# Performance work log

Measured on AMD Instinct MI355X. Metric: run time of the kernel, lower is better.

The kernel has to match this reference:

```python
import jax, jax.numpy as jnp
import numpy as np

L, B, S, D, H, F = 8, 8, 2048, 1024, 16, 4096
DH = D // H
EPS = 1e-5


def setup_inputs() -> dict:
    key = jax.random.key(0)
    ks = jax.random.split(key, 8)
    sc = 0.02
    return {
        "x": jax.random.normal(ks[0], (B, S, D), jnp.float32),
        "layer_indices": jax.random.randint(ks[1], (B,), 0, L, jnp.int32),
        "Wq": jax.random.normal(ks[2], (L, D, D), jnp.float32) * sc,
        "bq": jnp.zeros((L, D), jnp.float32),
        "Wk": jax.random.normal(ks[3], (L, D, D), jnp.float32) * sc,
        "bk": jnp.zeros((L, D), jnp.float32),
        "Wv": jax.random.normal(ks[4], (L, D, D), jnp.float32) * sc,
        "bv": jnp.zeros((L, D), jnp.float32),
        "Wo": jax.random.normal(ks[5], (L, D, D), jnp.float32) * sc,
        "bo": jnp.zeros((L, D), jnp.float32),
        "ln1_s": jnp.ones((L, D), jnp.float32),
        "ln1_b": jnp.zeros((L, D), jnp.float32),
        "ln2_s": jnp.ones((L, D), jnp.float32),
        "ln2_b": jnp.zeros((L, D), jnp.float32),
        "W1": jax.random.normal(ks[6], (L, D, F), jnp.float32) * sc,
        "b1": jnp.zeros((L, F), jnp.float32),
        "W2": jax.random.normal(ks[7], (L, F, D), jnp.float32) * sc,
        "b2": jnp.zeros((L, D), jnp.float32),
    }


def _layernorm(x, s, b):
    # x: [B,S,D]; s,b: [B,D] (per-routed-layer params)
    m = jnp.mean(x, axis=-1, keepdims=True)
    v = jnp.mean(jnp.square(x - m), axis=-1, keepdims=True)
    return (x - m) * jax.lax.rsqrt(v + EPS) * s[:, None, :] + b[:, None, :]


def reference(x, layer_indices, Wq, bq, Wk, bk, Wv, bv, Wo, bo,
              ln1_s, ln1_b, ln2_s, ln2_b, W1, b1, W2, b2):
    idx = layer_indices
    # Gather each batch element's routed layer parameters (MoE-style dispatch).
    Wq_g, bq_g = Wq[idx], bq[idx]
    Wk_g, bk_g = Wk[idx], bk[idx]
    Wv_g, bv_g = Wv[idx], bv[idx]
    Wo_g, bo_g = Wo[idx], bo[idx]
    s1, b1n = ln1_s[idx], ln1_b[idx]
    s2, b2n = ln2_s[idx], ln2_b[idx]
    W1_g, bf1 = W1[idx], b1[idx]
    W2_g, bf2 = W2[idx], b2[idx]

    # --- Multi-head self-attention (pre-LN) ---
    h = _layernorm(x, s1, b1n)                                   # [B,S,D]
    q = jnp.einsum('bsd,bde->bse', h, Wq_g) + bq_g[:, None, :]
    k = jnp.einsum('bsd,bde->bse', h, Wk_g) + bk_g[:, None, :]
    v = jnp.einsum('bsd,bde->bse', h, Wv_g) + bv_g[:, None, :]
    q = q.reshape(B, S, H, DH)
    k = k.reshape(B, S, H, DH)
    v = v.reshape(B, S, H, DH)
    scores = jnp.einsum('bqhd,bkhd->bhqk', q, k) / np.sqrt(DH)   # [B,H,S,S]
    probs = jax.nn.softmax(scores, axis=-1)
    attn = jnp.einsum('bhqk,bkhd->bqhd', probs, v).reshape(B, S, D)
    attn = jnp.einsum('bsd,bde->bse', attn, Wo_g) + bo_g[:, None, :]
    x = x + attn

    # --- Feed-forward (pre-LN) ---
    h = _layernorm(x, s2, b2n)
    h = jax.nn.gelu(jnp.einsum('bsd,bdf->bsf', h, W1_g) + bf1[:, None, :])
    h = jnp.einsum('bsf,bfd->bsd', h, W2_g) + bf2[:, None, :]
    return x + h
```

## Files before the change

kernel.cpp:

```cpp
#include <hip/hip_runtime.h>
#include <cstdint>
#include <cstddef>

typedef __attribute__((ext_vector_type(8))) short s8v;
typedef __attribute__((ext_vector_type(4))) float f4v;

constexpr int Lc = 8, Bc = 8, Sc = 2048, Dc = 1024, Hc = 16, Fc = 4096;

__device__ __forceinline__ unsigned short f2bf(float f) {
    unsigned int u = __float_as_uint(f);
    u = (u + 0x7FFFu + ((u >> 16) & 1u)) >> 16;
    return (unsigned short)u;
}

__device__ __forceinline__ void gload_lds16(const unsigned short* g, unsigned short* l) {
    __builtin_amdgcn_global_load_lds(
        (__attribute__((address_space(1))) void*)g,
        (__attribute__((address_space(3))) void*)l,
        16, 0, 0);
}

__global__ __launch_bounds__(256) void transpose_cast(
    const float* __restrict__ in, unsigned short* __restrict__ out, int R, int C) {
    __shared__ float tile[32][33];
    int l = blockIdx.z;
    int r0 = blockIdx.y << 5, c0 = blockIdx.x << 5;
    const float* ip = in + (size_t)l * R * C;
    unsigned short* op = out + (size_t)l * R * C;
    int tx = threadIdx.x & 31, ty = threadIdx.x >> 5;
#pragma unroll
    for (int i = 0; i < 4; i++)
        tile[ty + i * 8][tx] = ip[(size_t)(r0 + ty + i * 8) * C + (c0 + tx)];
    __syncthreads();
#pragma unroll
    for (int i = 0; i < 4; i++)
        op[(size_t)(c0 + ty + i * 8) * R + (r0 + tx)] = f2bf(tile[tx][ty + i * 8]);
}

__global__ __launch_bounds__(256) void ln_kernel(
    const float* __restrict__ x, const float* __restrict__ sc, const float* __restrict__ bi,
    const int* __restrict__ idx, unsigned short* __restrict__ out) {
    int row = blockIdx.x;
    int b = row >> 11;
    int l = idx[b];
    const float* xr = x + (size_t)row * Dc;
    int t = threadIdx.x;
    float4 xv = *(const float4*)(xr + t * 4);
    float s = xv.x + xv.y + xv.z + xv.w;
    float ss = xv.x * xv.x + xv.y * xv.y + xv.z * xv.z + xv.w * xv.w;
#pragma unroll
    for (int off = 32; off; off >>= 1) { s += __shfl_xor(s, off); ss += __shfl_xor(ss, off); }
    __shared__ float red[2][4];
    int w = t >> 6, lane = t & 63;
    if (lane == 0) { red[0][w] = s; red[1][w] = ss; }
    __syncthreads();
    float tot = red[0][0] + red[0][1] + red[0][2] + red[0][3];
    float tots = red[1][0] + red[1][1] + red[1][2] + red[1][3];
    float mean = tot * (1.0f / Dc);
    float var = tots * (1.0f / Dc) - mean * mean;
    float r = rsqrtf(var + 1e-5f);
    float4 s4 = *(const float4*)(sc + (size_t)l * Dc + t * 4);
    float4 b4 = *(const float4*)(bi + (size_t)l * Dc + t * 4);
    ushort4 o;
    o.x = f2bf((xv.x - mean) * r * s4.x + b4.x);
    o.y = f2bf((xv.y - mean) * r * s4.y + b4.y);
    o.z = f2bf((xv.z - mean) * r * s4.z + b4.z);
    o.w = f2bf((xv.w - mean) * r * s4.w + b4.w);
    *(ushort4*)(out + (size_t)row * Dc + t * 4) = o;
}

template <int EPI>
__global__ __launch_bounds__(256) void gemm_kernel(
    const unsigned short* __restrict__ A, const unsigned short* __restrict__ Wt,
    const float* __restrict__ bias, const int* __restrict__ idx,
    const float* __restrict__ resid, void* __restrict__ out, int M, int N, int K) {
    int b = blockIdx.z;
    int l = idx[b];
    int m0 = blockIdx.y << 7, n0 = blockIdx.x << 7;
    const unsigned short* Ab = A + (size_t)b * M * K;
    const unsigned short* Wl = Wt + (size_t)l * N * K;
    __shared__ alignas(16) unsigned short As[128][32];
    __shared__ alignas(16) unsigned short Bs[128][32];
    int tid = threadIdx.x, w = tid >> 6, lane = tid & 63, quad = lane >> 4, lr = lane & 15;
    int wm = (w >> 1) << 6, wn = (w & 1) << 6;
    f4v acc[4][4];
#pragma unroll
    for (int i = 0; i < 4; i++)
#pragma unroll
        for (int j = 0; j < 4; j++) acc[i][j] = 0.f;

    int chrow = 32 * w + (lane >> 2);
    int ks = (lane & 3) * 8;
    const unsigned short* agp0 = Ab + (size_t)(m0 + chrow) * K + ks;
    const unsigned short* agp1 = agp0 + (size_t)16 * K;
    const unsigned short* bgp0 = Wl + (size_t)(n0 + chrow) * K + ks;
    const unsigned short* bgp1 = bgp0 + (size_t)16 * K;
    unsigned short* lA0 = &As[32 * w][0];
    unsigned short* lA1 = &As[32 * w + 16][0];
    unsigned short* lB0 = &Bs[32 * w][0];
    unsigned short* lB1 = &Bs[32 * w + 16][0];

    for (int k0 = 0; k0 < K; k0 += 32) {
        gload_lds16(agp0, lA0);
        gload_lds16(agp1, lA1);
        gload_lds16(bgp0, lB0);
        gload_lds16(bgp1, lB1);
        agp0 += 32; agp1 += 32; bgp0 += 32; bgp1 += 32;
        __syncthreads();
        s8v af[4], bf[4];
#pragma unroll
        for (int i = 0; i < 4; i++) af[i] = *(const s8v*)&As[wm + i * 16 + lr][quad * 8];
#pragma unroll
        for (int j = 0; j < 4; j++) bf[j] = *(const s8v*)&Bs[wn + j * 16 + lr][quad * 8];
#pragma unroll
        for (int i = 0; i < 4; i++)
#pragma unroll
            for (int j = 0; j < 4; j++)
                acc[i][j] = __builtin_amdgcn_mfma_f32_16x16x32_bf16(af[i], bf[j], acc[i][j], 0, 0, 0);
        __syncthreads();
    }

    float bj[4];
#pragma unroll
    for (int j = 0; j < 4; j++) bj[j] = bias[(size_t)l * N + (n0 + wn + j * 16 + lr)];
    size_t obase = (size_t)b * M * N;
#pragma unroll
    for (int i = 0; i < 4; i++) {
#pragma unroll
        for (int r = 0; r < 4; r++) {
            int gm = m0 + wm + i * 16 + quad * 4 + r;
            size_t rowoff = obase + (size_t)gm * N;
#pragma unroll
            for (int j = 0; j < 4; j++) {
                int gn = n0 + wn + j * 16 + lr;
                float val = acc[i][j][r] + bj[j];
                if constexpr (EPI == 0) {
                    ((unsigned short*)out)[rowoff + gn] = f2bf(val);
                } else if constexpr (EPI == 1) {
                    float g = 0.5f * val * (1.0f + tanhf(0.7978845608f * (val + 0.044715f * val * val * val)));
                    ((unsigned short*)out)[rowoff + gn] = f2bf(g);
                } else {
                    ((float*)out)[rowoff + gn] = resid[rowoff + gn] + val;
                }
            }
        }
    }
}

__global__ __launch_bounds__(256) void flash_kernel(
    const unsigned short* __restrict__ qm, const unsigned short* __restrict__ km,
    const unsigned short* __restrict__ vm, unsigned short* __restrict__ om) {
    const int b = blockIdx.z, h = blockIdx.y, q0 = blockIdx.x << 6;
    const int tid = threadIdx.x, w = tid >> 6, lane = tid & 63, quad = lane >> 4, lr = lane & 15;
    __shared__ alignas(16) unsigned short Pl[4][16][72];
    __shared__ alignas(16) unsigned short Vt[64][72];
    const size_t bS = (size_t)b * Sc;
    const int hoff = h << 6;

    s8v aq0, aq1;
    {
        const unsigned short* qr = qm + (bS + q0 + w * 16 + lr) * (size_t)Dc + hoff;
        aq0 = *(const s8v*)(qr + quad * 8);
        aq1 = *(const s8v*)(qr + 32 + quad * 8);
    }
    f4v accO[4];
#pragma unroll
    for (int i = 0; i < 4; i++) accO[i] = 0.f;
    float m_i[4] = {-3e38f, -3e38f, -3e38f, -3e38f};
    float l_i[4] = {0.f, 0.f, 0.f, 0.f};

    const int vkey = tid >> 2, vc = tid & 3;

    for (int kv0 = 0; kv0 < Sc; kv0 += 64) {
        const unsigned short* vp = vm + (bS + kv0 + vkey) * (size_t)Dc + hoff + vc * 16;
        s8v v0 = *(const s8v*)vp;
        s8v v1 = *(const s8v*)(vp + 8);
        __syncthreads();
#pragma unroll
        for (int e = 0; e < 8; e++) {
            Vt[vc * 16 + e][vkey] = (unsigned short)v0[e];
            Vt[vc * 16 + 8 + e][vkey] = (unsigned short)v1[e];
        }
        f4v sc4[4];
#pragma unroll
        for (int j = 0; j < 4; j++) {
            const unsigned short* kr = km + (bS + kv0 + j * 16 + lr) * (size_t)Dc + hoff;
            s8v b0 = *(const s8v*)(kr + quad * 8);
            s8v b1 = *(const s8v*)(kr + 32 + quad * 8);
            f4v c = 0.f;
            c = __builtin_amdgcn_mfma_f32_16x16x32_bf16(aq0, b0, c, 0, 0, 0);
            c = __builtin_amdgcn_mfma_f32_16x16x32_bf16(aq1, b1, c, 0, 0, 0);
            sc4[j] = c * 0.125f;
        }
        float alpha[4], pmat[4][4];
#pragma unroll
        for (int rr = 0; rr < 4; rr++) {
            float lm = fmaxf(fmaxf(sc4[0][rr], sc4[1][rr]), fmaxf(sc4[2][rr], sc4[3][rr]));
#pragma unroll
            for (int off = 1; off < 16; off <<= 1) lm = fmaxf(lm, __shfl_xor(lm, off));
            float mn = fmaxf(m_i[rr], lm);
            alpha[rr] = __expf(m_i[rr] - mn);
            m_i[rr] = mn;
            float ls = 0.f;
#pragma unroll
            for (int j = 0; j < 4; j++) {
                float p = __expf(sc4[j][rr] - mn);
                pmat[j][rr] = p;
                ls += p;
            }
#pragma unroll
            for (int off = 1; off < 16; off <<= 1) ls += __shfl_xor(ls, off);
            l_i[rr] = l_i[rr] * alpha[rr] + ls;
        }
#pragma unroll
        for (int jd = 0; jd < 4; jd++)
#pragma unroll
            for (int rr = 0; rr < 4; rr++) accO[jd][rr] *= alpha[rr];
#pragma unroll
        for (int j = 0; j < 4; j++)
#pragma unroll
            for (int rr = 0; rr < 4; rr++)
                Pl[w][quad * 4 + rr][j * 16 + lr] = f2bf(pmat[j][rr]);
        __syncthreads();
        s8v ap0 = *(const s8v*)&Pl[w][lr][quad * 8];
        s8v ap1 = *(const s8v*)&Pl[w][lr][32 + quad * 8];
#pragma unroll
        for (int jd = 0; jd < 4; jd++) {
            s8v b0 = *(const s8v*)&Vt[jd * 16 + lr][quad * 8];
            s8v b1 = *(const s8v*)&Vt[jd * 16 + lr][32 + quad * 8];
            accO[jd] = __builtin_amdgcn_mfma_f32_16x16x32_bf16(ap0, b0, accO[jd], 0, 0, 0);
            accO[jd] = __builtin_amdgcn_mfma_f32_16x16x32_bf16(ap1, b1, accO[jd], 0, 0, 0);
        }
    }
#pragma unroll
    for (int jd = 0; jd < 4; jd++)
#pragma unroll
        for (int rr = 0; rr < 4; rr++)
            om[(bS + q0 + w * 16 + quad * 4 + rr) * (size_t)Dc + hoff + jd * 16 + lr] =
                f2bf(accO[jd][rr] / l_i[rr]);
}

extern "C" void kernel_launch(void* const* d_in, const int* in_sizes, int n_in,
                              void* d_out, int out_size, void* d_ws, size_t ws_size,
                              hipStream_t stream) {
    const float* x  = (const float*)d_in[0];
    const int* idx  = (const int*)d_in[1];
    const float* Wq = (const float*)d_in[2];  const float* bq  = (const float*)d_in[3];
    const float* Wk = (const float*)d_in[4];  const float* bk  = (const float*)d_in[5];
    const float* Wv = (const float*)d_in[6];  const float* bv  = (const float*)d_in[7];
    const float* Wo = (const float*)d_in[8];  const float* bo  = (const float*)d_in[9];
    const float* s1 = (const float*)d_in[10]; const float* b1n = (const float*)d_in[11];
    const float* s2 = (const float*)d_in[12]; const float* b2n = (const float*)d_in[13];
    const float* W1 = (const float*)d_in[14]; const float* bf1 = (const float*)d_in[15];
    const float* W2 = (const float*)d_in[16]; const float* bf2 = (const float*)d_in[17];

    const size_t eDD  = (size_t)Lc * Dc * Dc;
    const size_t eDF  = (size_t)Lc * Dc * Fc;
    const size_t eBSD = (size_t)Bc * Sc * Dc;
    unsigned short* Wtq = (unsigned short*)d_ws;
    unsigned short* Wtk = Wtq + eDD;
    unsigned short* Wtv = Wtk + eDD;
    unsigned short* Wto = Wtv + eDD;
    unsigned short* Wt1 = Wto + eDD;
    unsigned short* Wt2 = Wt1 + eDF;
    unsigned short* hb  = Wt2 + eDF;
    unsigned short* qb  = hb + eBSD;
    unsigned short* kb  = qb + eBSD;
    unsigned short* vb  = kb + eBSD;
    unsigned short* ab  = vb + eBSD;
    float* x2           = (float*)(ab + eBSD);
    unsigned short* fb  = qb;

    dim3 blk(256);
    transpose_cast<<<dim3(Dc / 32, Dc / 32, Lc), blk, 0, stream>>>(Wq, Wtq, Dc, Dc);
    transpose_cast<<<dim3(Dc / 32, Dc / 32, Lc), blk, 0, stream>>>(Wk, Wtk, Dc, Dc);
    transpose_cast<<<dim3(Dc / 32, Dc / 32, Lc), blk, 0, stream>>>(Wv, Wtv, Dc, Dc);
    transpose_cast<<<dim3(Dc / 32, Dc / 32, Lc), blk, 0, stream>>>(Wo, Wto, Dc, Dc);
    transpose_cast<<<dim3(Fc / 32, Dc / 32, Lc), blk, 0, stream>>>(W1, Wt1, Dc, Fc);
    transpose_cast<<<dim3(Dc / 32, Fc / 32, Lc), blk, 0, stream>>>(W2, Wt2, Fc, Dc);
    ln_kernel<<<Bc * Sc, blk, 0, stream>>>(x, s1, b1n, idx, hb);
    gemm_kernel<0><<<dim3(Dc / 128, Sc / 128, Bc), blk, 0, stream>>>(hb, Wtq, bq, idx, nullptr, qb, Sc, Dc, Dc);
    gemm_kernel<0><<<dim3(Dc / 128, Sc / 128, Bc), blk, 0, stream>>>(hb, Wtk, bk, idx, nullptr, kb, Sc, Dc, Dc);
    gemm_kernel<0><<<dim3(Dc / 128, Sc / 128, Bc), blk, 0, stream>>>(hb, Wtv, bv, idx, nullptr, vb, Sc, Dc, Dc);
    flash_kernel<<<dim3(Sc / 64, Hc, Bc), blk, 0, stream>>>(qb, kb, vb, ab);
    gemm_kernel<2><<<dim3(Dc / 128, Sc / 128, Bc), blk, 0, stream>>>(ab, Wto, bo, idx, x, x2, Sc, Dc, Dc);
    ln_kernel<<<Bc * Sc, blk, 0, stream>>>(x2, s2, b2n, idx, hb);
    gemm_kernel<1><<<dim3(Fc / 128, Sc / 128, Bc), blk, 0, stream>>>(hb, Wt1, bf1, idx, nullptr, fb, Sc, Fc, Dc);
    gemm_kernel<2><<<dim3(Dc / 128, Sc / 128, Bc), blk, 0, stream>>>(fb, Wt2, bf2, idx, x2, (float*)d_out, Sc, Dc, Fc);
}
```

Baseline: 1.789 ms.

## Produce V transposed from its projection GEMM and read it directly in flash attention

The V projection GEMM now runs with the weight as the left operand, so V is written head-dim-major ([B, D, S]) and the bias is applied per output row. The flash kernel then loads the V operand straight from global memory in MFMA layout, which removes the per-tile LDS transpose and the two block-wide barriers. The cost is that V fragments are read from global/L2 by every wave rather than once per block into shared memory, and the V GEMM's epilogue stores run along S.

New measurement: 2.141 ms. +19.7%, slower.

```diff
diff --git a/kernel.cpp b/kernel.cpp
--- a/kernel.cpp
+++ b/kernel.cpp
@@ -69,7 +69,7 @@
     *(ushort4*)(out + (size_t)row * Dc + t * 4) = o;
 }
 
-template <int EPI>
+template <int EPI, bool WLEFT = false>
 __global__ __launch_bounds__(256) void gemm_kernel(
     const unsigned short* __restrict__ A, const unsigned short* __restrict__ Wt,
     const float* __restrict__ bias, const int* __restrict__ idx,
@@ -77,8 +77,8 @@
     int b = blockIdx.z;
     int l = idx[b];
     int m0 = blockIdx.y << 7, n0 = blockIdx.x << 7;
-    const unsigned short* Ab = A + (size_t)b * M * K;
-    const unsigned short* Wl = Wt + (size_t)l * N * K;
+    const unsigned short* Ab = A + (WLEFT ? (size_t)l : (size_t)b) * M * K;
+    const unsigned short* Wl = Wt + (WLEFT ? (size_t)b : (size_t)l) * N * K;
     __shared__ alignas(16) unsigned short As[128][32];
     __shared__ alignas(16) unsigned short Bs[128][32];
     int tid = threadIdx.x, w = tid >> 6, lane = tid & 63, quad = lane >> 4, lr = lane & 15;
@@ -121,8 +121,10 @@
     }
 
     float bj[4];
-#pragma unroll
-    for (int j = 0; j < 4; j++) bj[j] = bias[(size_t)l * N + (n0 + wn + j * 16 + lr)];
+    if constexpr (!WLEFT) {
+#pragma unroll
+        for (int j = 0; j < 4; j++) bj[j] = bias[(size_t)l * N + (n0 + wn + j * 16 + lr)];
+    }
     size_t obase = (size_t)b * M * N;
 #pragma unroll
     for (int i = 0; i < 4; i++) {
@@ -130,10 +132,12 @@
         for (int r = 0; r < 4; r++) {
             int gm = m0 + wm + i * 16 + quad * 4 + r;
             size_t rowoff = obase + (size_t)gm * N;
+            float bm;
+            if constexpr (WLEFT) bm = bias[(size_t)l * M + gm];
 #pragma unroll
             for (int j = 0; j < 4; j++) {
                 int gn = n0 + wn + j * 16 + lr;
-                float val = acc[i][j][r] + bj[j];
+                float val = acc[i][j][r] + (WLEFT ? bm : bj[j]);
                 if constexpr (EPI == 0) {
                     ((unsigned short*)out)[rowoff + gn] = f2bf(val);
                 } else if constexpr (EPI == 1) {
@@ -153,9 +157,9 @@
     const int b = blockIdx.z, h = blockIdx.y, q0 = blockIdx.x << 6;
     const int tid = threadIdx.x, w = tid >> 6, lane = tid & 63, quad = lane >> 4, lr = lane & 15;
     __shared__ alignas(16) unsigned short Pl[4][16][72];
-    __shared__ alignas(16) unsigned short Vt[64][72];
     const size_t bS = (size_t)b * Sc;
     const int hoff = h << 6;
+    const unsigned short* vtb = vm + ((size_t)b * Dc + hoff) * Sc;
 
     s8v aq0, aq1;
     {
@@ -169,18 +173,7 @@
     float m_i[4] = {-3e38f, -3e38f, -3e38f, -3e38f};
     float l_i[4] = {0.f, 0.f, 0.f, 0.f};
 
-    const int vkey = tid >> 2, vc = tid & 3;
-
     for (int kv0 = 0; kv0 < Sc; kv0 += 64) {
-        const unsigned short* vp = vm + (bS + kv0 + vkey) * (size_t)Dc + hoff + vc * 16;
-        s8v v0 = *(const s8v*)vp;
-        s8v v1 = *(const s8v*)(vp + 8);
-        __syncthreads();
-#pragma unroll
-        for (int e = 0; e < 8; e++) {
-            Vt[vc * 16 + e][vkey] = (unsigned short)v0[e];
-            Vt[vc * 16 + 8 + e][vkey] = (unsigned short)v1[e];
-        }
         f4v sc4[4];
 #pragma unroll
         for (int j = 0; j < 4; j++) {
@@ -221,13 +214,13 @@
 #pragma unroll
             for (int rr = 0; rr < 4; rr++)
                 Pl[w][quad * 4 + rr][j * 16 + lr] = f2bf(pmat[j][rr]);
-        __syncthreads();
         s8v ap0 = *(const s8v*)&Pl[w][lr][quad * 8];
         s8v ap1 = *(const s8v*)&Pl[w][lr][32 + quad * 8];
 #pragma unroll
         for (int jd = 0; jd < 4; jd++) {
-            s8v b0 = *(const s8v*)&Vt[jd * 16 + lr][quad * 8];
-            s8v b1 = *(const s8v*)&Vt[jd * 16 + lr][32 + quad * 8];
+            const unsigned short* vr = vtb + (size_t)(jd * 16 + lr) * Sc + kv0;
+            s8v b0 = *(const s8v*)(vr + quad * 8);
+            s8v b1 = *(const s8v*)(vr + 32 + quad * 8);
             accO[jd] = __builtin_amdgcn_mfma_f32_16x16x32_bf16(ap0, b0, accO[jd], 0, 0, 0);
             accO[jd] = __builtin_amdgcn_mfma_f32_16x16x32_bf16(ap1, b1, accO[jd], 0, 0, 0);
         }
@@ -281,7 +274,7 @@
     ln_kernel<<<Bc * Sc, blk, 0, stream>>>(x, s1, b1n, idx, hb);
     gemm_kernel<0><<<dim3(Dc / 128, Sc / 128, Bc), blk, 0, stream>>>(hb, Wtq, bq, idx, nullptr, qb, Sc, Dc, Dc);
     gemm_kernel<0><<<dim3(Dc / 128, Sc / 128, Bc), blk, 0, stream>>>(hb, Wtk, bk, idx, nullptr, kb, Sc, Dc, Dc);
-    gemm_kernel<0><<<dim3(Dc / 128, Sc / 128, Bc), blk, 0, stream>>>(hb, Wtv, bv, idx, nullptr, vb, Sc, Dc, Dc);
+    gemm_kernel<0, true><<<dim3(Sc / 128, Dc / 128, Bc), blk, 0, stream>>>(Wtv, hb, bv, idx, nullptr, vb, Dc, Sc, Dc);
     flash_kernel<<<dim3(Sc / 64, Hc, Bc), blk, 0, stream>>>(qb, kb, vb, ab);
     gemm_kernel<2><<<dim3(Dc / 128, Sc / 128, Bc), blk, 0, stream>>>(ab, Wto, bo, idx, x, x2, Sc, Dc, Dc);
     ln_kernel<<<Bc * Sc, blk, 0, stream>>>(x2, s2, b2n, idx, hb);
```
